# Performance work log

Measured on AMD Instinct MI355X. Metric: run time of the kernel, lower is better.

## Reference

```python
import jax, jax.numpy as jnp
import numpy as np

B, N, L, H, V, LAYERS = 512, 32, 50, 256, 100000, 1


def setup_inputs() -> dict:
    key = jax.random.key(0)
    ks = jax.random.split(key, 18)
    std = 1.0 / np.sqrt(H)
    u = lambda k, shape: jax.random.uniform(k, shape, jnp.float32, -std, std)
    return {
        # forward args
        "A": jax.random.uniform(ks[0], (B, N, 2 * N), jnp.float32),
        "items": jax.random.randint(ks[1], (B, N), 0, V + 1),
        "seq_alias": jax.random.randint(ks[2], (B, L), 0, N),
        "mask": jnp.ones((B, L), jnp.int32),
        # learned parameters (uniform(-1/sqrt(H), 1/sqrt(H)) as in the module)
        "emb": u(ks[3], (V + 1, H)),
        "W_in": u(ks[4], (H, H)), "b_in": u(ks[5], (H,)),
        "W_out": u(ks[6], (H, H)), "b_out": u(ks[7], (H,)),
        "W_ih": u(ks[8], (2 * H, 3 * H)), "b_ih": u(ks[9], (3 * H,)),
        "W_hh": u(ks[10], (H, 3 * H)), "b_hh": u(ks[11], (3 * H,)),
        "fc1_w": u(ks[12], (H, H)), "fc1_b": u(ks[13], (H,)),
        "fc2_w": u(ks[14], (H, H)), "fc2_b": u(ks[15], (H,)),
        "fc3_w": u(ks[16], (H, 1)),
    }


def reference(A, items, seq_alias, mask, emb, W_in, b_in, W_out, b_out,
              W_ih, b_ih, W_hh, b_hh, fc1_w, fc1_b, fc2_w, fc2_b, fc3_w):
    # --- GGNN over dense batched adjacency A: [B, N, 2N] ---
    h = emb[items]  # [B, N, H]
    for _ in range(LAYERS):
        m_in = jnp.einsum('bij,bjh->bih', A[:, :, :N], h @ W_in + b_in)
        m_out = jnp.einsum('bij,bjh->bih', A[:, :, N:], h @ W_out + b_out)
        a = jnp.concatenate([m_in, m_out], axis=-1)  # [B, N, 2H]
        # torch.nn.GRUCell math
        gi = a @ W_ih + b_ih  # [B, N, 3H]
        gh = h @ W_hh + b_hh
        i_r, i_z, i_n = jnp.split(gi, 3, axis=-1)
        h_r, h_z, h_n = jnp.split(gh, 3, axis=-1)
        r = jax.nn.sigmoid(i_r + h_r)
        z = jax.nn.sigmoid(i_z + h_z)
        ng = jnp.tanh(i_n + r * h_n)
        h = ng + z * (h - ng)
    # --- per-sample gather of session sequences (vectorized embed_seq) ---
    h_seqs = jnp.take_along_axis(h, seq_alias[:, :, None], axis=1)  # [B, L, H]
    tail = mask.sum(axis=1) - 1  # index of last valid position
    h_tail = jnp.take_along_axis(h_seqs, tail[:, None, None], axis=1)[:, 0]  # [B, H]
    # --- attention pooling ---
    q1 = (h_tail @ fc1_w + fc1_b)[:, None, :]  # [B, 1, H]
    q2 = h_seqs @ fc2_w + fc2_b                # [B, L, H]
    alpha = jax.nn.sigmoid(q1 + q2) @ fc3_w    # [B, L, 1]
    seq_emb = jnp.sum(alpha * h_seqs * mask[:, :, None].astype(h.dtype), axis=1)  # [B, H]
    # --- score against all items (excluding padding row 0) ---
    return seq_emb @ emb[1:].T  # [B, V]
```

## Files before the change

### kernel.cpp

```cpp
#include <hip/hip_runtime.h>
#include <cmath>

#define HH 256
#define NB 32
#define LSEQ 50
#define BB 512
#define VOC 100000

typedef __attribute__((ext_vector_type(8))) short short8;
typedef __attribute__((ext_vector_type(4))) float f32x4;

static __device__ __forceinline__ unsigned short f2bf(float x) {
  unsigned u = __builtin_bit_cast(unsigned, x);
  u = (u + 0x7fff + ((u >> 16) & 1)) >> 16;
  return (unsigned short)u;
}
static __device__ __forceinline__ float bf2f(unsigned short h) {
  unsigned u = ((unsigned)h) << 16;
  return __builtin_bit_cast(float, u);
}
static __device__ __forceinline__ uint2 pack_hi4(float4 x, uint2& pl) {
  const unsigned short h0 = f2bf(x.x), h1 = f2bf(x.y), h2 = f2bf(x.z), h3 = f2bf(x.w);
  const unsigned short l0 = f2bf(x.x - bf2f(h0)), l1 = f2bf(x.y - bf2f(h1));
  const unsigned short l2 = f2bf(x.z - bf2f(h2)), l3 = f2bf(x.w - bf2f(h3));
  uint2 ph;
  ph.x = (unsigned)h0 | ((unsigned)h1 << 16);
  ph.y = (unsigned)h2 | ((unsigned)h3 << 16);
  pl.x = (unsigned)l0 | ((unsigned)l1 << 16);
  pl.y = (unsigned)l2 | ((unsigned)l3 << 16);
  return ph;
}

__global__ void prep_weights(const float* __restrict__ W_in, const float* __restrict__ b_in,
                             const float* __restrict__ W_out, const float* __restrict__ b_out,
                             const float* __restrict__ W_hh, const float* __restrict__ b_hh,
                             const float* __restrict__ W_ih, const float* __restrict__ fc2_w,
                             unsigned short* __restrict__ Wt_all, float* __restrict__ b_all,
                             unsigned short* __restrict__ WihT, unsigned short* __restrict__ fc2T)
{
  const int bid = blockIdx.x, k = threadIdx.x;
  if (bid < 1280) {
    const float* src; const float* bsrc; int col, nc;
    if (bid < 256)      { src = W_in;  bsrc = b_in;  col = bid;       nc = 256; }
    else if (bid < 512) { src = W_out; bsrc = b_out; col = bid - 256; nc = 256; }
    else                { src = W_hh;  bsrc = b_hh;  col = bid - 512; nc = 768; }
    Wt_all[bid * 256 + k] = f2bf(src[k * nc + col]);
    if (k == 0) b_all[bid] = bsrc[col];
  } else if (bid < 2048) {
    const int n = bid - 1280;
    WihT[n * 512 + k]       = f2bf(W_ih[k * 768 + n]);
    WihT[n * 512 + k + 256] = f2bf(W_ih[(k + 256) * 768 + n]);
  } else {
    const int n = bid - 2048;
    fc2T[n * 256 + k] = f2bf(fc2_w[k * 256 + n]);
  }
}

__global__ __launch_bounds__(256, 3) void gemm_asplit_nt(
    const unsigned short* __restrict__ Ah, const unsigned short* __restrict__ Al,
    const unsigned short* __restrict__ Bt, const float* __restrict__ bias,
    float* __restrict__ C, int N, int K, int ldc)
{
  __shared__ unsigned short sAh[4 * 128 * 8];
  __shared__ unsigned short sAl[4 * 128 * 8];
  __shared__ unsigned short sB [4 * 128 * 8];
  const int tid = threadIdx.x;
  const int n0 = blockIdx.x * 128, m0 = blockIdx.y * 128;
  const int lane = tid & 63, wave = tid >> 6;
  const int quad = lane >> 4, l16 = lane & 15;
  const int wm = (wave >> 1) * 64, wn = (wave & 1) * 64;

  f32x4 acc[4][4];
#pragma unroll
  for (int i = 0; i < 4; ++i)
#pragma unroll
    for (int j = 0; j < 4; ++j)
#pragma unroll
      for (int r = 0; r < 4; ++r) acc[i][j][r] = 0.f;

  const int c0 = tid, c1 = tid + 256;
  const int q0 = c0 >> 7, r0 = c0 & 127;
  const int q1c = c1 >> 7, r1 = c1 & 127;

  for (int k0 = 0; k0 < K; k0 += 32) {
    const size_t ga0 = (size_t)(m0 + r0) * K + k0 + q0 * 8;
    const size_t ga1 = (size_t)(m0 + r1) * K + k0 + q1c * 8;
    const size_t gb0 = (size_t)(n0 + r0) * K + k0 + q0 * 8;
    const size_t gb1 = (size_t)(n0 + r1) * K + k0 + q1c * 8;
    *(uint4*)&sAh[c0 * 8] = *(const uint4*)&Ah[ga0];
    *(uint4*)&sAh[c1 * 8] = *(const uint4*)&Ah[ga1];
    *(uint4*)&sAl[c0 * 8] = *(const uint4*)&Al[ga0];
    *(uint4*)&sAl[c1 * 8] = *(const uint4*)&Al[ga1];
    *(uint4*)&sB [c0 * 8] = *(const uint4*)&Bt[gb0];
    *(uint4*)&sB [c1 * 8] = *(const uint4*)&Bt[gb1];
    __syncthreads();

    short8 fah[4], fal[4];
#pragma unroll
    for (int ms = 0; ms < 4; ++ms) {
      const int row = wm + ms * 16 + l16;
      fah[ms] = *(const short8*)&sAh[(quad * 128 + row) * 8];
      fal[ms] = *(const short8*)&sAl[(quad * 128 + row) * 8];
    }
#pragma unroll
    for (int ns = 0; ns < 4; ++ns) {
      const int col = wn + ns * 16 + l16;
      const short8 fb = *(const short8*)&sB[(quad * 128 + col) * 8];
#pragma unroll
      for (int ms = 0; ms < 4; ++ms) {
        acc[ms][ns] = __builtin_amdgcn_mfma_f32_16x16x32_bf16(fah[ms], fb, acc[ms][ns], 0, 0, 0);
        acc[ms][ns] = __builtin_amdgcn_mfma_f32_16x16x32_bf16(fal[ms], fb, acc[ms][ns], 0, 0, 0);
      }
    }
    __syncthreads();
  }

#pragma unroll
  for (int ns = 0; ns < 4; ++ns) {
    const int n = n0 + wn + ns * 16 + l16;
    const float bv = bias[n];
#pragma unroll
    for (int ms = 0; ms < 4; ++ms) {
      const int mrow = m0 + wm + ms * 16 + quad * 4;
#pragma unroll
      for (int r = 0; r < 4; ++r)
        C[(size_t)(mrow + r) * ldc + n] = acc[ms][ns][r] + bv;
    }
  }
}

#define TS 64
#define KSTEP 16
#define LDPF 68
__global__ __launch_bounds__(256) void gemm_nn_bias(
    const float* __restrict__ A, const float* __restrict__ W,
    const float* __restrict__ bias, float* __restrict__ C,
    int M, int N, int K)
{
  __shared__ float As[KSTEP * LDPF];
  __shared__ float Ws[KSTEP * LDPF];
  const int tid = threadIdx.x;
  const int tx = tid & 15, ty = tid >> 4;
  const int n0 = blockIdx.x * TS, m0 = blockIdx.y * TS;
  const int lkk = tid & 15, lm = tid >> 4;
  const int ln  = tid & 63, lkr = tid >> 6;
  float acc[4][4] = {};
  for (int k0 = 0; k0 < K; k0 += KSTEP) {
#pragma unroll
    for (int r = 0; r < 4; ++r)
      As[lkk * LDPF + lm + r * 16] = A[(m0 + lm + r * 16) * K + k0 + lkk];
#pragma unroll
    for (int r = 0; r < 4; ++r)
      Ws[(lkr + r * 4) * LDPF + ln] = W[(k0 + lkr + r * 4) * N + n0 + ln];
    __syncthreads();
#pragma unroll
    for (int kk = 0; kk < KSTEP; ++kk) {
      const float4 a4 = *(const float4*)(As + kk * LDPF + ty * 4);
      const float4 w4 = *(const float4*)(Ws + kk * LDPF + tx * 4);
      const float av[4] = {a4.x, a4.y, a4.z, a4.w};
      const float wv[4] = {w4.x, w4.y, w4.z, w4.w};
#pragma unroll
      for (int i = 0; i < 4; ++i)
#pragma unroll
        for (int j = 0; j < 4; ++j)
          acc[i][j] += av[i] * wv[j];
    }
    __syncthreads();
  }
  const float4 b4 = *(const float4*)(bias + n0 + tx * 4);
  const float bv[4] = {b4.x, b4.y, b4.z, b4.w};
#pragma unroll
  for (int i = 0; i < 4; ++i) {
    float4 o;
    o.x = acc[i][0] + bv[0]; o.y = acc[i][1] + bv[1];
    o.z = acc[i][2] + bv[2]; o.w = acc[i][3] + bv[3];
    *(float4*)(C + (m0 + ty * 4 + i) * N + n0 + tx * 4) = o;
  }
}

__global__ void gather_h0(const int* __restrict__ items, const float* __restrict__ emb,
                          float* __restrict__ h0, unsigned short* __restrict__ h0h,
                          unsigned short* __restrict__ h0l, int total4)
{
  const int e = blockIdx.x * blockDim.x + threadIdx.x;
  if (e >= total4) return;
  const int row = e >> 6, c = e & 63;
  const int it = items[row];
  const float4 x = ((const float4*)emb)[it * 64 + c];
  ((float4*)h0)[e] = x;
  uint2 pl;
  const uint2 ph = pack_hi4(x, pl);
  *(uint2*)&h0h[e * 4] = ph;
  *(uint2*)&h0l[e * 4] = pl;
}

__global__ __launch_bounds__(256) void msg_kernel(
    const float* __restrict__ A, const float* __restrict__ C1,
    unsigned short* __restrict__ ach, unsigned short* __restrict__ acl)
{
  const int b = blockIdx.x;
  const int tid = threadIdx.x;
  __shared__ float Ash[NB * 64];
#pragma unroll
  for (int r = 0; r < 8; ++r)
    Ash[tid + r * 256] = A[b * (NB * 2 * NB) + tid + r * 256];
  float hi[NB], ho[NB];
#pragma unroll
  for (int j = 0; j < NB; ++j) {
    hi[j] = C1[(size_t)(b * NB + j) * 1280 + tid];
    ho[j] = C1[(size_t)(b * NB + j) * 1280 + 256 + tid];
  }
  __syncthreads();
  for (int i = 0; i < NB; ++i) {
    float si = 0.f, so = 0.f;
#pragma unroll
    for (int j = 0; j < NB; ++j) {
      si += Ash[i * 64 + j] * hi[j];
      so += Ash[i * 64 + 32 + j] * ho[j];
    }
    const int idx = (b * NB + i) * 512 + tid;
    const unsigned short sh = f2bf(si);
    ach[idx] = sh; acl[idx] = f2bf(si - bf2f(sh));
    const unsigned short oh = f2bf(so);
    ach[idx + 256] = oh; acl[idx + 256] = f2bf(so - bf2f(oh));
  }
}

__global__ void gru_kernel(const float* __restrict__ gi, const float* __restrict__ C1,
                           float* __restrict__ h, int total)
{
  const int idx = blockIdx.x * blockDim.x + threadIdx.x;
  if (idx >= total) return;
  const int row = idx >> 8, k = idx & 255;
  const float* gir = gi + (size_t)row * 768;
  const float* ghr = C1 + (size_t)row * 1280 + 512;
  const float ir = gir[k], iz = gir[k + 256], inn = gir[k + 512];
  const float hr = ghr[k], hz = ghr[k + 256], hn = ghr[k + 512];
  const float r = 1.f / (1.f + expf(-(ir + hr)));
  const float z = 1.f / (1.f + expf(-(iz + hz)));
  const float n = tanhf(inn + r * hn);
  const float h0v = h[idx];
  h[idx] = n + z * (h0v - n);
}

__global__ __launch_bounds__(256) void seq_gather(
    const int* __restrict__ seq_alias, const int* __restrict__ mask,
    const float* __restrict__ h, float* __restrict__ h_seqs,
    unsigned short* __restrict__ hsh, unsigned short* __restrict__ hsl,
    float* __restrict__ h_tail)
{
  const int b = blockIdx.x, tid = threadIdx.x;
  __shared__ int tail_sh;
  if (tid == 0) {
    int s = 0;
    for (int l = 0; l < LSEQ; ++l) s += mask[b * LSEQ + l];
    tail_sh = s - 1;
  }
  __syncthreads();
  const int tail = tail_sh;
  for (int l = 0; l < LSEQ; ++l) {
    const int al = seq_alias[b * LSEQ + l];
    const float v = h[(size_t)(b * NB + al) * HH + tid];
    const int idx = (b * LSEQ + l) * HH + tid;
    h_seqs[idx] = v;
    const unsigned short vh = f2bf(v);
    hsh[idx] = vh; hsl[idx] = f2bf(v - bf2f(vh));
    if (l == tail) h_tail[b * HH + tid] = v;
  }
}

__global__ __launch_bounds__(256) void attn_kernel(
    const float* __restrict__ q1, const float* __restrict__ q2,
    const float* __restrict__ fc3_w, const float* __restrict__ h_seqs,
    const int* __restrict__ mask, float* __restrict__ seq_emb)
{
  const int b = blockIdx.x, k = threadIdx.x;
  __shared__ float red[4];
  __shared__ float alpha_sh;
  const float q1k = q1[b * HH + k];
  const float w3 = fc3_w[k];
  float acc = 0.f;
  for (int l = 0; l < LSEQ; ++l) {
    const float q2v = q2[(size_t)(b * LSEQ + l) * HH + k];
    float v = (1.f / (1.f + expf(-(q1k + q2v)))) * w3;
#pragma unroll
    for (int off = 32; off > 0; off >>= 1) v += __shfl_down(v, off, 64);
    if ((k & 63) == 0) red[k >> 6] = v;
    __syncthreads();
    if (k == 0) alpha_sh = red[0] + red[1] + red[2] + red[3];
    __syncthreads();
    const float alpha = alpha_sh;
    if (mask[b * LSEQ + l]) acc += alpha * h_seqs[(size_t)(b * LSEQ + l) * HH + k];
  }
  seq_emb[b * HH + k] = acc;
}

__global__ void split_seq(const float* __restrict__ s, unsigned short* __restrict__ hi,
                          unsigned short* __restrict__ lo, int n)
{
  const int i = blockIdx.x * blockDim.x + threadIdx.x;
  if (i >= n) return;
  const float x = s[i];
  const unsigned short h = f2bf(x);
  hi[i] = h;
  lo[i] = f2bf(x - bf2f(h));
}

#define ELD2 136
__global__ __launch_bounds__(256, 3) void scorer_mfma(
    const unsigned short* __restrict__ seq_hi,
    const unsigned short* __restrict__ seq_lo,
    const float* __restrict__ emb,
    float* __restrict__ out)
{
  __shared__ unsigned short ehi[64 * ELD2];
  __shared__ unsigned short elo[64 * ELD2];
  const int tid = threadIdx.x;
  const int v0 = blockIdx.x * 64;
  const int m0 = blockIdx.y * 256;
  const int lane = tid & 63, wave = tid >> 6;
  const int quad = lane >> 4, l16 = lane & 15;
  const int mwave = m0 + wave * 64;

  f32x4 acc[4][4];
#pragma unroll
  for (int i = 0; i < 4; ++i)
#pragma unroll
    for (int j = 0; j < 4; ++j)
#pragma unroll
      for (int r = 0; r < 4; ++r) acc[i][j][r] = 0.f;

  for (int p = 0; p < 2; ++p) {
#pragma unroll
    for (int i = 0; i < 8; ++i) {
      const int idx4 = tid + i * 256;
      const int row = idx4 >> 5, c4 = idx4 & 31;
      const int v = v0 + row;
      float4 x = make_float4(0.f, 0.f, 0.f, 0.f);
      if (v < VOC) x = *(const float4*)&emb[(size_t)(v + 1) * HH + p * 128 + c4 * 4];
      uint2 pl;
      const uint2 ph = pack_hi4(x, pl);
      *(uint2*)&ehi[row * ELD2 + c4 * 4] = ph;
      *(uint2*)&elo[row * ELD2 + c4 * 4] = pl;
    }
    __syncthreads();

#pragma unroll
    for (int ks = 0; ks < 4; ++ks) {
      const int kk = ks * 32;
      short8 bh[4], bl[4];
#pragma unroll
      for (int vs = 0; vs < 4; ++vs) {
        const int off = (vs * 16 + l16) * ELD2 + kk + quad * 8;
        bh[vs] = *(const short8*)&ehi[off];
        bl[vs] = *(const short8*)&elo[off];
      }
#pragma unroll
      for (int ms = 0; ms < 4; ++ms) {
        const int m = mwave + ms * 16 + l16;
        const int aoff = m * HH + p * 128 + kk + quad * 8;
        const short8 ah = *(const short8*)&seq_hi[aoff];
        const short8 al = *(const short8*)&seq_lo[aoff];
#pragma unroll
        for (int vs = 0; vs < 4; ++vs) {
          acc[ms][vs] = __builtin_amdgcn_mfma_f32_16x16x32_bf16(ah, bh[vs], acc[ms][vs], 0, 0, 0);
          acc[ms][vs] = __builtin_amdgcn_mfma_f32_16x16x32_bf16(ah, bl[vs], acc[ms][vs], 0, 0, 0);
          acc[ms][vs] = __builtin_amdgcn_mfma_f32_16x16x32_bf16(al, bh[vs], acc[ms][vs], 0, 0, 0);
        }
      }
    }
    __syncthreads();
  }

#pragma unroll
  for (int ms = 0; ms < 4; ++ms) {
    const int mrow = mwave + ms * 16 + quad * 4;
#pragma unroll
    for (int vs = 0; vs < 4; ++vs) {
      const int v = v0 + vs * 16 + l16;
      if (v < VOC) {
#pragma unroll
        for (int r = 0; r < 4; ++r)
          out[(size_t)(mrow + r) * VOC + v] = acc[ms][vs][r];
      }
    }
  }
}

extern "C" void kernel_launch(void* const* d_in, const int* in_sizes, int n_in,
                              void* d_out, int out_size, void* d_ws, size_t ws_size,
                              hipStream_t stream)
{
  const float* A      = (const float*)d_in[0];
  const int* items    = (const int*)d_in[1];
  const int* seq_al   = (const int*)d_in[2];
  const int* mask     = (const int*)d_in[3];
  const float* emb    = (const float*)d_in[4];
  const float* W_in   = (const float*)d_in[5];
  const float* b_in   = (const float*)d_in[6];
  const float* W_out  = (const float*)d_in[7];
  const float* b_out  = (const float*)d_in[8];
  const float* W_ih   = (const float*)d_in[9];
  const float* b_ih   = (const float*)d_in[10];
  const float* W_hh   = (const float*)d_in[11];
  const float* b_hh   = (const float*)d_in[12];
  const float* fc1_w  = (const float*)d_in[13];
  const float* fc1_b  = (const float*)d_in[14];
  const float* fc2_w  = (const float*)d_in[15];
  const float* fc2_b  = (const float*)d_in[16];
  const float* fc3_w  = (const float*)d_in[17];
  float* out = (float*)d_out;

  float* ws = (float*)d_ws;
  float* h0      = ws;
  float* q1      = ws + 4194304;
  float* h_tail  = ws + 4325376;
  float* seq_emb = ws + 4456448;
  unsigned short* seq_hi = (unsigned short*)(ws + 4587520);
  unsigned short* seq_lo = (unsigned short*)(ws + 4653056);
  unsigned short* Wt_all = (unsigned short*)(ws + 4718592);
  unsigned short* WihT   = (unsigned short*)(ws + 4882432);
  unsigned short* fc2T   = (unsigned short*)(ws + 5079040);
  float* b_all   = ws + 5111808;

  float* C1 = out;
  unsigned short* acat_h = (unsigned short*)(out + 20971520);
  unsigned short* acat_l = (unsigned short*)(out + 25165824);
  float* gi = out + 29360128;
  unsigned short* h0h = (unsigned short*)(out + 41943040);
  unsigned short* h0l = (unsigned short*)(out + 44040192);
  float* h_seqs = out;
  unsigned short* hs_h = (unsigned short*)(out + 6553600);
  unsigned short* hs_l = (unsigned short*)(out + 9830400);
  float* q2 = out + 13107200;

  const int MR = BB * NB;

  prep_weights<<<dim3(2304), dim3(256), 0, stream>>>(
      W_in, b_in, W_out, b_out, W_hh, b_hh, W_ih, fc2_w, Wt_all, b_all, WihT, fc2T);

  gather_h0<<<dim3(MR * 64 / 256), dim3(256), 0, stream>>>(items, emb, h0, h0h, h0l, MR * 64);

  gemm_asplit_nt<<<dim3(1280 / 128, MR / 128), dim3(256), 0, stream>>>(
      h0h, h0l, Wt_all, b_all, C1, 1280, 256, 1280);

  msg_kernel<<<dim3(BB), dim3(256), 0, stream>>>(A, C1, acat_h, acat_l);

  gemm_asplit_nt<<<dim3(768 / 128, MR / 128), dim3(256), 0, stream>>>(
      acat_h, acat_l, WihT, b_ih, gi, 768, 512, 768);

  gru_kernel<<<dim3(MR * HH / 256), dim3(256), 0, stream>>>(gi, C1, h0, MR * HH);

  seq_gather<<<dim3(BB), dim3(256), 0, stream>>>(seq_al, mask, h0, h_seqs, hs_h, hs_l, h_tail);

  gemm_asplit_nt<<<dim3(256 / 128, (BB * LSEQ) / 128), dim3(256), 0, stream>>>(
      hs_h, hs_l, fc2T, fc2_b, q2, 256, 256, 256);

  gemm_nn_bias<<<dim3(HH / TS, BB / TS), dim3(256), 0, stream>>>(h_tail, fc1_w, fc1_b, q1, BB, HH, HH);

  attn_kernel<<<dim3(BB), dim3(256), 0, stream>>>(q1, q2, fc3_w, h_seqs, mask, seq_emb);

  split_seq<<<dim3(BB * HH / 256), dim3(256), 0, stream>>>(seq_emb, seq_hi, seq_lo, BB * HH);

  scorer_mfma<<<dim3((VOC + 63) / 64, 2), dim3(256), 0, stream>>>(seq_hi, seq_lo, emb, out);
}
```

Baseline: 710.8 us.

## Pre-split embeddings for scorer, use direct-to-LDS loads, and parallelize gather/attention

Adds an embsplit pass that converts the embedding table once into padded bf16 hi/lo arrays. A new scorer reads these directly from global memory into MFMA fragments, without per-block conversion and LDS staging. The GEMM tile loads switch to global_load_lds direct copies. seq_gather is split across 5 blocks per batch with a wave-reduced mask sum, and attention gives one sequence position per wave with no per-step block syncs. The presplit path needs extra workspace (about 100 MB) and adds a full-table conversion pass per call, with a fallback to the old scorer when workspace is too small.

```diff
diff --git a/kernel.cpp b/kernel.cpp
--- a/kernel.cpp
+++ b/kernel.cpp
@@ -6,6 +6,7 @@
 #define LSEQ 50
 #define BB 512
 #define VOC 100000
+#define VPAD 100032
 
 typedef __attribute__((ext_vector_type(8))) short short8;
 typedef __attribute__((ext_vector_type(4))) float f32x4;
@@ -29,6 +30,12 @@
   pl.x = (unsigned)l0 | ((unsigned)l1 << 16);
   pl.y = (unsigned)l2 | ((unsigned)l3 << 16);
   return ph;
+}
+
+static __device__ __forceinline__ void cp16(void* lds, const void* g) {
+  __builtin_amdgcn_global_load_lds(
+      (const __attribute__((address_space(1))) unsigned int*)g,
+      (__attribute__((address_space(3))) unsigned int*)lds, 16, 0, 0);
 }
 
 __global__ void prep_weights(const float* __restrict__ W_in, const float* __restrict__ b_in,
@@ -56,6 +63,20 @@
   }
 }
 
+__global__ __launch_bounds__(256) void embsplit(const float* __restrict__ emb,
+                                                unsigned short* __restrict__ ehi,
+                                                unsigned short* __restrict__ elo)
+{
+  const int idx4 = blockIdx.x * 256 + threadIdx.x;
+  const int v = idx4 >> 6, c4 = idx4 & 63;
+  float4 x = make_float4(0.f, 0.f, 0.f, 0.f);
+  if (v < VOC) x = *(const float4*)&emb[(size_t)(v + 1) * HH + c4 * 4];
+  uint2 pl;
+  const uint2 ph = pack_hi4(x, pl);
+  *(uint2*)&ehi[(size_t)v * HH + c4 * 4] = ph;
+  *(uint2*)&elo[(size_t)v * HH + c4 * 4] = pl;
+}
+
 __global__ __launch_bounds__(256, 3) void gemm_asplit_nt(
     const unsigned short* __restrict__ Ah, const unsigned short* __restrict__ Al,
     const unsigned short* __restrict__ Bt, const float* __restrict__ bias,
@@ -87,12 +108,12 @@
     const size_t ga1 = (size_t)(m0 + r1) * K + k0 + q1c * 8;
     const size_t gb0 = (size_t)(n0 + r0) * K + k0 + q0 * 8;
     const size_t gb1 = (size_t)(n0 + r1) * K + k0 + q1c * 8;
-    *(uint4*)&sAh[c0 * 8] = *(const uint4*)&Ah[ga0];
-    *(uint4*)&sAh[c1 * 8] = *(const uint4*)&Ah[ga1];
-    *(uint4*)&sAl[c0 * 8] = *(const uint4*)&Al[ga0];
-    *(uint4*)&sAl[c1 * 8] = *(const uint4*)&Al[ga1];
-    *(uint4*)&sB [c0 * 8] = *(const uint4*)&Bt[gb0];
-    *(uint4*)&sB [c1 * 8] = *(const uint4*)&Bt[gb1];
+    cp16(&sAh[c0 * 8], &Ah[ga0]);
+    cp16(&sAh[c1 * 8], &Ah[ga1]);
+    cp16(&sAl[c0 * 8], &Al[ga0]);
+    cp16(&sAl[c1 * 8], &Al[ga1]);
+    cp16(&sB [c0 * 8], &Bt[gb0]);
+    cp16(&sB [c1 * 8], &Bt[gb1]);
     __syncthreads();
 
     short8 fah[4], fal[4];
@@ -243,7 +264,7 @@
   h[idx] = n + z * (h0v - n);
 }
 
-__global__ __launch_bounds__(256) void seq_gather(
+__global__ __launch_bounds__(256) void seq_gather2(
     const int* __restrict__ seq_alias, const int* __restrict__ mask,
     const float* __restrict__ h, float* __restrict__ h_seqs,
     unsigned short* __restrict__ hsh, unsigned short* __restrict__ hsl,
@@ -251,14 +272,16 @@
 {
   const int b = blockIdx.x, tid = threadIdx.x;
   __shared__ int tail_sh;
-  if (tid == 0) {
-    int s = 0;
-    for (int l = 0; l < LSEQ; ++l) s += mask[b * LSEQ + l];
-    tail_sh = s - 1;
+  if (tid < 64) {
+    int s = (tid < LSEQ) ? mask[b * LSEQ + tid] : 0;
+#pragma unroll
+    for (int off = 32; off > 0; off >>= 1) s += __shfl_down(s, off, 64);
+    if (tid == 0) tail_sh = s - 1;
   }
   __syncthreads();
   const int tail = tail_sh;
-  for (int l = 0; l < LSEQ; ++l) {
+  const int l0 = blockIdx.y * 10;
+  for (int l = l0; l < l0 + 10; ++l) {
     const int al = seq_alias[b * LSEQ + l];
     const float v = h[(size_t)(b * NB + al) * HH + tid];
     const int idx = (b * LSEQ + l) * HH + tid;
@@ -269,30 +292,33 @@
   }
 }
 
-__global__ __launch_bounds__(256) void attn_kernel(
+__global__ __launch_bounds__(256) void attn_kernel2(
     const float* __restrict__ q1, const float* __restrict__ q2,
     const float* __restrict__ fc3_w, const float* __restrict__ h_seqs,
     const int* __restrict__ mask, float* __restrict__ seq_emb)
 {
-  const int b = blockIdx.x, k = threadIdx.x;
-  __shared__ float red[4];
-  __shared__ float alpha_sh;
-  const float q1k = q1[b * HH + k];
-  const float w3 = fc3_w[k];
-  float acc = 0.f;
-  for (int l = 0; l < LSEQ; ++l) {
-    const float q2v = q2[(size_t)(b * LSEQ + l) * HH + k];
-    float v = (1.f / (1.f + expf(-(q1k + q2v)))) * w3;
-#pragma unroll
-    for (int off = 32; off > 0; off >>= 1) v += __shfl_down(v, off, 64);
-    if ((k & 63) == 0) red[k >> 6] = v;
-    __syncthreads();
-    if (k == 0) alpha_sh = red[0] + red[1] + red[2] + red[3];
-    __syncthreads();
-    const float alpha = alpha_sh;
-    if (mask[b * LSEQ + l]) acc += alpha * h_seqs[(size_t)(b * LSEQ + l) * HH + k];
-  }
-  seq_emb[b * HH + k] = acc;
+  const int b = blockIdx.x;
+  const int tid = threadIdx.x, wave = tid >> 6, lane = tid & 63;
+  __shared__ float red[4 * HH];
+  const float4 q1v = *(const float4*)&q1[b * HH + lane * 4];
+  const float4 w3v = *(const float4*)&fc3_w[lane * 4];
+  float4 acc = make_float4(0.f, 0.f, 0.f, 0.f);
+  for (int l = wave; l < LSEQ; l += 4) {
+    if (!mask[b * LSEQ + l]) continue;
+    const float4 q2v = *(const float4*)&q2[(size_t)(b * LSEQ + l) * HH + lane * 4];
+    float s = (1.f / (1.f + expf(-(q1v.x + q2v.x)))) * w3v.x
+            + (1.f / (1.f + expf(-(q1v.y + q2v.y)))) * w3v.y
+            + (1.f / (1.f + expf(-(q1v.z + q2v.z)))) * w3v.z
+            + (1.f / (1.f + expf(-(q1v.w + q2v.w)))) * w3v.w;
+#pragma unroll
+    for (int off = 32; off > 0; off >>= 1) s += __shfl_xor(s, off, 64);
+    const float4 hv = *(const float4*)&h_seqs[(size_t)(b * LSEQ + l) * HH + lane * 4];
+    acc.x += s * hv.x; acc.y += s * hv.y; acc.z += s * hv.z; acc.w += s * hv.w;
+  }
+  *(float4*)&red[wave * HH + lane * 4] = acc;
+  __syncthreads();
+  const float r = red[tid] + red[HH + tid] + red[2 * HH + tid] + red[3 * HH + tid];
+  seq_emb[b * HH + tid] = r;
 }
 
 __global__ void split_seq(const float* __restrict__ s, unsigned short* __restrict__ hi,
@@ -304,6 +330,67 @@
   const unsigned short h = f2bf(x);
   hi[i] = h;
   lo[i] = f2bf(x - bf2f(h));
+}
+
+__global__ __launch_bounds__(256, 4) void scorer_presplit(
+    const unsigned short* __restrict__ seq_hi,
+    const unsigned short* __restrict__ seq_lo,
+    const unsigned short* __restrict__ ehi,
+    const unsigned short* __restrict__ elo,
+    float* __restrict__ out)
+{
+  const int tid = threadIdx.x;
+  const int m0 = blockIdx.x * 256;
+  const int v0 = blockIdx.y * 64;
+  const int lane = tid & 63, wave = tid >> 6;
+  const int quad = lane >> 4, l16 = lane & 15;
+  const int mwave = m0 + wave * 64;
+
+  f32x4 acc[4][4];
+#pragma unroll
+  for (int i = 0; i < 4; ++i)
+#pragma unroll
+    for (int j = 0; j < 4; ++j)
+#pragma unroll
+      for (int r = 0; r < 4; ++r) acc[i][j][r] = 0.f;
+
+#pragma unroll
+  for (int ks = 0; ks < 8; ++ks) {
+    const int kk = ks * 32 + quad * 8;
+    short8 bh[4], bl[4];
+#pragma unroll
+    for (int vs = 0; vs < 4; ++vs) {
+      const int boff = (v0 + vs * 16 + l16) * HH + kk;
+      bh[vs] = *(const short8*)&ehi[boff];
+      bl[vs] = *(const short8*)&elo[boff];
+    }
+#pragma unroll
+    for (int ms = 0; ms < 4; ++ms) {
+      const int aoff = (mwave + ms * 16 + l16) * HH + kk;
+      const short8 ah = *(const short8*)&seq_hi[aoff];
+      const short8 al = *(const short8*)&seq_lo[aoff];
+#pragma unroll
+      for (int vs = 0; vs < 4; ++vs) {
+        acc[ms][vs] = __builtin_amdgcn_mfma_f32_16x16x32_bf16(ah, bh[vs], acc[ms][vs], 0, 0, 0);
+        acc[ms][vs] = __builtin_amdgcn_mfma_f32_16x16x32_bf16(ah, bl[vs], acc[ms][vs], 0, 0, 0);
+        acc[ms][vs] = __builtin_amdgcn_mfma_f32_16x16x32_bf16(al, bh[vs], acc[ms][vs], 0, 0, 0);
+      }
+    }
+  }
+
+#pragma unroll
+  for (int ms = 0; ms < 4; ++ms) {
+    const int mrow = mwave + ms * 16 + quad * 4;
+#pragma unroll
+    for (int vs = 0; vs < 4; ++vs) {
+      const int v = v0 + vs * 16 + l16;
+      if (v < VOC) {
+#pragma unroll
+        for (int r = 0; r < 4; ++r)
+          out[(size_t)(mrow + r) * VOC + v] = acc[ms][vs][r];
+      }
+    }
+  }
 }
 
 #define ELD2 136
@@ -422,6 +509,9 @@
   unsigned short* WihT   = (unsigned short*)(ws + 4882432);
   unsigned short* fc2T   = (unsigned short*)(ws + 5079040);
   float* b_all   = ws + 5111808;
+  unsigned short* emb_hi = (unsigned short*)(ws + 5113088);
+  unsigned short* emb_lo = (unsigned short*)(ws + 5113088 + (size_t)VPAD * HH / 2);
+  const bool presplit = ws_size >= ((size_t)5113088 * 4 + (size_t)VPAD * HH * 4);
 
   float* C1 = out;
   unsigned short* acat_h = (unsigned short*)(out + 20971520);
@@ -439,6 +529,9 @@
   prep_weights<<<dim3(2304), dim3(256), 0, stream>>>(
       W_in, b_in, W_out, b_out, W_hh, b_hh, W_ih, fc2_w, Wt_all, b_all, WihT, fc2T);
 
+  if (presplit)
+    embsplit<<<dim3(VPAD * 64 / 256), dim3(256), 0, stream>>>(emb, emb_hi, emb_lo);
+
   gather_h0<<<dim3(MR * 64 / 256), dim3(256), 0, stream>>>(items, emb, h0, h0h, h0l, MR * 64);
 
   gemm_asplit_nt<<<dim3(1280 / 128, MR / 128), dim3(256), 0, stream>>>(
@@ -451,16 +544,20 @@
 
   gru_kernel<<<dim3(MR * HH / 256), dim3(256), 0, stream>>>(gi, C1, h0, MR * HH);
 
-  seq_gather<<<dim3(BB), dim3(256), 0, stream>>>(seq_al, mask, h0, h_seqs, hs_h, hs_l, h_tail);
+  seq_gather2<<<dim3(BB, 5), dim3(256), 0, stream>>>(seq_al, mask, h0, h_seqs, hs_h, hs_l, h_tail);
 
   gemm_asplit_nt<<<dim3(256 / 128, (BB * LSEQ) / 128), dim3(256), 0, stream>>>(
       hs_h, hs_l, fc2T, fc2_b, q2, 256, 256, 256);
 
   gemm_nn_bias<<<dim3(HH / TS, BB / TS), dim3(256), 0, stream>>>(h_tail, fc1_w, fc1_b, q1, BB, HH, HH);
 
-  attn_kernel<<<dim3(BB), dim3(256), 0, stream>>>(q1, q2, fc3_w, h_seqs, mask, seq_emb);
+  attn_kernel2<<<dim3(BB), dim3(256), 0, stream>>>(q1, q2, fc3_w, h_seqs, mask, seq_emb);
 
   split_seq<<<dim3(BB * HH / 256), dim3(256), 0, stream>>>(seq_emb, seq_hi, seq_lo, BB * HH);
 
-  scorer_mfma<<<dim3((VOC + 63) / 64, 2), dim3(256), 0, stream>>>(seq_hi, seq_lo, emb, out);
-}
+  if (presplit)
+    scorer_presplit<<<dim3(2, (VOC + 63) / 64), dim3(256), 0, stream>>>(
+        seq_hi, seq_lo, emb_hi, emb_lo, out);
+  else
+    scorer_mfma<<<dim3((VOC + 63) / 64, 2), dim3(256), 0, stream>>>(seq_hi, seq_lo, emb, out);
+}
```

New measurement: 778.6 us. +9.5%, slower.
